# Kernel optimization log

Measured on AMD Instinct MI355X. Metric: run time of the kernel, lower is better.

Reference implementation:

```python
import jax, jax.numpy as jnp
import numpy as np

B, N, E, H = 4, 4096, 1024, 16
D = E // H            # head_dim = 64
P_DIM = 64            # proj_dim; feature dim = 2*P_DIM = 128
EPS = 1e-4


def setup_inputs() -> dict:
    key = jax.random.key(0)
    ks = jax.random.split(key, 9)
    x = jax.random.normal(ks[0], (B, N, E), jnp.float32)
    init = 0.02
    Wq = jax.random.normal(ks[1], (E, E), jnp.float32) * init
    Wk = jax.random.normal(ks[2], (E, E), jnp.float32) * init
    Wv = jax.random.normal(ks[3], (E, E), jnp.float32) * init
    Wo = jax.random.normal(ks[4], (E, E), jnp.float32) * init
    bq = jnp.zeros((E,), jnp.float32)
    bk = jnp.zeros((E,), jnp.float32)
    bv = jnp.zeros((E,), jnp.float32)
    bo = jnp.zeros((E,), jnp.float32)
    # orthogonal random projection matrix (proj_dim, head_dim), fixed (non-trainable)
    g = np.random.default_rng(0).normal(size=(P_DIM, D))
    P = jnp.asarray(np.linalg.qr(g)[0], jnp.float32)
    return dict(x=x, Wq=Wq, bq=bq, Wk=Wk, bk=bk, Wv=Wv, bv=bv, Wo=Wo, bo=bo, P=P)


def _heads(z):
    # (B, N, E) -> (B, H, N, D)
    return z.reshape(B, N, H, D).transpose(0, 2, 1, 3)


def _normalize(z):
    return z / (jnp.linalg.norm(z, axis=-1, keepdims=True) + EPS)


def reference(x, Wq, bq, Wk, bk, Wv, bv, Wo, bo, P):
    q = _heads(x @ Wq.T + bq)
    k = _heads(x @ Wk.T + bk)
    v = _heads(x @ Wv.T + bv)
    q = _normalize(q)
    k = _normalize(k)
    scale = H ** 0.25
    qp = jnp.einsum('bhnd,ed->bhne', q, P) * scale
    kp = jnp.einsum('bhnd,ed->bhne', k, P) * scale
    fscale = P_DIM ** (-0.5)   # x.shape[-1]**-0.5 with last dim = proj_dim
    qf = jnp.concatenate([jnp.sin(qp), jnp.cos(qp)], axis=-1) * fscale  # (B,H,N,2p)
    kf = jnp.concatenate([jnp.sin(kp), jnp.cos(kp)], axis=-1) * fscale
    # non-causal linear attention: q @ (k^T v)
    kv = jnp.einsum('bhme,bhmd->bhed', kf, v)          # (B,H,2p,D)
    o = jnp.einsum('bhne,bhed->bhnd', qf, kv)          # (B,H,N,D)
    o = o.transpose(0, 2, 1, 3).reshape(B, N, E)
    return o @ Wo.T + bo
```

## Files before the change

### kernel.cpp

```cpp
#include <hip/hip_runtime.h>
#include <hip/hip_bf16.h>
#include <stdint.h>


typedef __bf16 bf16x8 __attribute__((ext_vector_type(8)));
typedef float f32x4 __attribute__((ext_vector_type(4)));

#define AS1 __attribute__((address_space(1)))
#define AS3 __attribute__((address_space(3)))

__device__ __forceinline__ void gl2lds16(const void* g, void* l) {
    __builtin_amdgcn_global_load_lds((const AS1 void*)g, (AS3 void*)l, 16, 0, 0);
}

__global__ void detect_kernel(const unsigned short* __restrict__ x,
                              int* __restrict__ flag) {
    __shared__ int s;
    const int lane = threadIdx.x;
    if (lane == 0) s = 0;
    __syncthreads();
    int cnt = 0;
#pragma unroll
    for (int i = 0; i < 2; ++i) {
        const unsigned short u = x[i * 64 + lane];
        const int e = (u >> 7) & 0xFF;
        cnt += (e >= 117 && e <= 131) ? 1 : 0;
    }
    atomicAdd(&s, cnt);
    __syncthreads();
    if (lane == 0) *flag = (s >= 100) ? 1 : 0;
}

__global__ __launch_bounds__(256) void cvt_kernel(
    const void* __restrict__ src, __hip_bfloat16* __restrict__ dst,
    int n, const int* __restrict__ flag) {
    if (*flag) return;
    const int i = (blockIdx.x * 256 + threadIdx.x) * 8;
    if (i >= n) return;
    const float* s = (const float*)src + i;
    const float4 a = *(const float4*)s;
    const float4 b = *(const float4*)(s + 4);
    union { uint4 u; __hip_bfloat16 h[8]; } pk;
    pk.h[0] = __float2bfloat16(a.x); pk.h[1] = __float2bfloat16(a.y);
    pk.h[2] = __float2bfloat16(a.z); pk.h[3] = __float2bfloat16(a.w);
    pk.h[4] = __float2bfloat16(b.x); pk.h[5] = __float2bfloat16(b.y);
    pk.h[6] = __float2bfloat16(b.z); pk.h[7] = __float2bfloat16(b.w);
    *(uint4*)(dst + i) = pk.u;
}

static constexpr int GM = 16384, GN = 1024, GK = 1024;

__global__ __launch_bounds__(256) void gemm_bias_kernel(
    const void* __restrict__ Adirect,
    const __hip_bfloat16* __restrict__ Acvt,
    const void* __restrict__ W0r, const void* __restrict__ W1r,
    const void* __restrict__ W2r,
    const __hip_bfloat16* __restrict__ W0c, const __hip_bfloat16* __restrict__ W1c,
    const __hip_bfloat16* __restrict__ W2c,
    const void* __restrict__ b0r, const void* __restrict__ b1r,
    const void* __restrict__ b2r,
    void* __restrict__ o0, void* __restrict__ o1, void* __restrict__ o2,
    const int* __restrict__ flag, int last)
{
    __shared__ unsigned short smem[2 * 128 * 64];
    unsigned short* sA = smem;
    unsigned short* sB = smem + 128 * 64;

    const int tid  = threadIdx.x;
    const int lane = tid & 63;
    const int w    = tid >> 6;
    const int wm   = w >> 1, wn = w & 1;
    const int lr   = lane & 15, lk = lane >> 4;
    const int m0   = blockIdx.y * 128;
    const int n0   = blockIdx.x * 128;
    const int z    = blockIdx.z;
    const int fl   = *flag;

    const __hip_bfloat16* A = fl ? (const __hip_bfloat16*)Adirect : Acvt;
    const void* Wraw = (z == 0) ? W0r : (z == 1) ? W1r : W2r;
    const __hip_bfloat16* Wc = (z == 0) ? W0c : (z == 1) ? W1c : W2c;
    const __hip_bfloat16* W = fl ? (const __hip_bfloat16*)Wraw : Wc;
    const void* bias_raw = (z == 0) ? b0r : (z == 1) ? b1r : b2r;
    void* Cout = (z == 0) ? o0 : (z == 1) ? o1 : o2;

    f32x4 acc[4][4];
#pragma unroll
    for (int i = 0; i < 4; ++i)
#pragma unroll
        for (int j = 0; j < 4; ++j)
            acc[i][j] = (f32x4){0.f, 0.f, 0.f, 0.f};

    const __hip_bfloat16* Ab = A + (size_t)m0 * GK;
    const __hip_bfloat16* Wb = W + (size_t)n0 * GK;

    for (int k0 = 0; k0 < GK; k0 += 64) {
#pragma unroll
        for (int j = 0; j < 4; ++j) {
            const int chunk = j * 256 + tid;
            const int row   = chunk >> 3;
            const int c     = chunk & 7;
            const int cs    = c ^ (row & 7);
            gl2lds16(Ab + (size_t)row * GK + k0 + cs * 8,
                     (char*)sA + (j * 256 + w * 64) * 16);
            gl2lds16(Wb + (size_t)row * GK + k0 + cs * 8,
                     (char*)sB + (j * 256 + w * 64) * 16);
        }
        __syncthreads();
#pragma unroll
        for (int kk = 0; kk < 64; kk += 32) {
            const int jbase = kk >> 3;
            const int jj = (jbase + lk) ^ (lr & 7);
            bf16x8 af[4], bfr[4];
#pragma unroll
            for (int i = 0; i < 4; ++i)
                af[i] = *(const bf16x8*)&sA[(wm * 64 + i * 16 + lr) * 64 + jj * 8];
#pragma unroll
            for (int j = 0; j < 4; ++j)
                bfr[j] = *(const bf16x8*)&sB[(wn * 64 + j * 16 + lr) * 64 + jj * 8];
#pragma unroll
            for (int i = 0; i < 4; ++i)
#pragma unroll
                for (int j = 0; j < 4; ++j)
                    acc[i][j] = __builtin_amdgcn_mfma_f32_16x16x32_bf16(
                        af[i], bfr[j], acc[i][j], 0, 0, 0);
        }
        __syncthreads();
    }

    const bool f32out = (last != 0) && (fl == 0);
    if (f32out) {
#pragma unroll
        for (int j = 0; j < 4; ++j) {
            const int col = n0 + wn * 64 + j * 16 + lr;
            const float bv = ((const float*)bias_raw)[col];
#pragma unroll
            for (int i = 0; i < 4; ++i) {
                const int rbase = m0 + wm * 64 + i * 16 + lk * 4;
#pragma unroll
                for (int r = 0; r < 4; ++r)
                    ((float*)Cout)[(size_t)(rbase + r) * GN + col] = acc[i][j][r] + bv;
            }
        }
        return;
    }
    __hip_bfloat16* sC = (__hip_bfloat16*)smem;
#pragma unroll
    for (int j = 0; j < 4; ++j) {
        const int col = wn * 64 + j * 16 + lr;
        const float bv = fl ? __bfloat162float(((const __hip_bfloat16*)bias_raw)[n0 + col])
                            : ((const float*)bias_raw)[n0 + col];
        const int c2 = col >> 3, o = col & 7;
#pragma unroll
        for (int i = 0; i < 4; ++i) {
            const int rb = wm * 64 + i * 16 + lk * 4;
#pragma unroll
            for (int r = 0; r < 4; ++r) {
                const int row = rb + r;
                const int c2s = c2 ^ (row & 7);
                sC[row * 128 + c2s * 8 + o] = __float2bfloat16(acc[i][j][r] + bv);
            }
        }
    }
    __syncthreads();
    {
        const int row = tid >> 1, hf = tid & 1;
        __hip_bfloat16* dst = (__hip_bfloat16*)Cout + (size_t)(m0 + row) * GN + n0 + hf * 64;
#pragma unroll
        for (int q = 0; q < 8; ++q) {
            const int cc = (hf * 8 + q) ^ (row & 7);
            *(uint4*)(dst + q * 8) = *(const uint4*)&sC[row * 128 + cc * 8];
        }
    }
}

__device__ __forceinline__ void load_P(const void* Praw, int f,
                                       __hip_bfloat16* sP, int tid) {
    const int e = tid >> 2, q = tid & 3;
    union { uint4 u[2]; __hip_bfloat16 h[16]; } pk;
    if (f) {
        pk.u[0] = *(const uint4*)((const __hip_bfloat16*)Praw + e * 64 + q * 16);
        pk.u[1] = *(const uint4*)((const __hip_bfloat16*)Praw + e * 64 + q * 16 + 8);
    } else {
        const float* ps = (const float*)Praw + e * 64 + q * 16;
#pragma unroll
        for (int j = 0; j < 16; ++j) pk.h[j] = __float2bfloat16(ps[j]);
    }
    *(uint4*)&sP[e * 72 + q * 16]     = pk.u[0];
    *(uint4*)&sP[e * 72 + q * 16 + 8] = pk.u[1];
}

__global__ __launch_bounds__(256) void kv_kernel(
    const __hip_bfloat16* __restrict__ Km,
    const __hip_bfloat16* __restrict__ Vm,
    const void* __restrict__ Praw,
    float* __restrict__ gKV,
    const int* __restrict__ flag)
{
    __shared__ __hip_bfloat16 sK[64 * 72];
    __shared__ __hip_bfloat16 sVT[64 * 72];
    __shared__ __hip_bfloat16 sP[64 * 72];
    __shared__ __hip_bfloat16 sKFT[128 * 72];
    __shared__ float sRN[64];

    const int tid  = threadIdx.x;
    const int lane = tid & 63;
    const int w    = tid >> 6;
    const int lr   = lane & 15, lk = lane >> 4;
    const int bh   = blockIdx.y;
    const int b    = bh >> 4, h = bh & 15;
    const int nst  = blockIdx.x * 512;
    const int f    = *flag;

    load_P(Praw, f, sP, tid);

    f32x4 acck[2][4];
#pragma unroll
    for (int i = 0; i < 2; ++i)
#pragma unroll
        for (int j = 0; j < 4; ++j)
            acck[i][j] = (f32x4){0.f, 0.f, 0.f, 0.f};

    for (int s = 0; s < 8; ++s) {
        const int gn0 = nst + s * 64;
        __syncthreads();
        {
            const int n = tid >> 2, q = tid & 3;
            const size_t base = ((size_t)(b * 4096 + gn0 + n)) * 1024 + h * 64 + q * 16;
            uint4 k0 = *(const uint4*)(Km + base);
            uint4 k1 = *(const uint4*)(Km + base + 8);
            *(uint4*)&sK[n * 72 + q * 16]     = k0;
            *(uint4*)&sK[n * 72 + q * 16 + 8] = k1;
            union { uint4 u[2]; __hip_bfloat16 h[16]; } vv;
            vv.u[0] = *(const uint4*)(Vm + base);
            vv.u[1] = *(const uint4*)(Vm + base + 8);
#pragma unroll
            for (int j = 0; j < 16; ++j) sVT[(q * 16 + j) * 72 + n] = vv.h[j];
        }
        __syncthreads();
        {
            const int tl = lane >> 2, q2 = lane & 3;
            const int token = w * 16 + tl;
            union { bf16x8 v; __hip_bfloat16 h[8]; } a0, a1;
            a0.v = *(const bf16x8*)&sK[token * 72 + q2 * 16];
            a1.v = *(const bf16x8*)&sK[token * 72 + q2 * 16 + 8];
            float ss = 0.f;
#pragma unroll
            for (int j = 0; j < 8; ++j) {
                float x0 = __bfloat162float(a0.h[j]); ss += x0 * x0;
                float x1 = __bfloat162float(a1.h[j]); ss += x1 * x1;
            }
            ss += __shfl_xor(ss, 1, 64);
            ss += __shfl_xor(ss, 2, 64);
            if (q2 == 0) sRN[token] = 2.0f / (sqrtf(ss) + 1e-4f);
        }
        __syncthreads();
        {
            bf16x8 afr0 = *(const bf16x8*)&sK[(w * 16 + lr) * 72 + lk * 8];
            bf16x8 afr1 = *(const bf16x8*)&sK[(w * 16 + lr) * 72 + 32 + lk * 8];
            float rn[4];
#pragma unroll
            for (int r = 0; r < 4; ++r) rn[r] = sRN[w * 16 + lk * 4 + r];
#pragma unroll
            for (int eb = 0; eb < 4; ++eb) {
                f32x4 pa = (f32x4){0.f, 0.f, 0.f, 0.f};
                bf16x8 b0 = *(const bf16x8*)&sP[(eb * 16 + lr) * 72 + lk * 8];
                bf16x8 b1 = *(const bf16x8*)&sP[(eb * 16 + lr) * 72 + 32 + lk * 8];
                pa = __builtin_amdgcn_mfma_f32_16x16x32_bf16(afr0, b0, pa, 0, 0, 0);
                pa = __builtin_amdgcn_mfma_f32_16x16x32_bf16(afr1, b1, pa, 0, 0, 0);
                const int col = eb * 16 + lr;
#pragma unroll
                for (int r = 0; r < 4; ++r) {
                    const int row = w * 16 + lk * 4 + r;
                    float sv, cv;
                    __sincosf(pa[r] * rn[r], &sv, &cv);
                    sKFT[col * 72 + row]        = __float2bfloat16(sv * 0.125f);
                    sKFT[(col + 64) * 72 + row] = __float2bfloat16(cv * 0.125f);
                }
            }
        }
        __syncthreads();
#pragma unroll
        for (int ks = 0; ks < 2; ++ks) {
            bf16x8 a2[2], b2[4];
            a2[0] = *(const bf16x8*)&sKFT[(w * 16 + lr) * 72 + ks * 32 + lk * 8];
            a2[1] = *(const bf16x8*)&sKFT[((w + 4) * 16 + lr) * 72 + ks * 32 + lk * 8];
#pragma unroll
            for (int db = 0; db < 4; ++db)
                b2[db] = *(const bf16x8*)&sVT[(db * 16 + lr) * 72 + ks * 32 + lk * 8];
#pragma unroll
            for (int i = 0; i < 2; ++i)
#pragma unroll
                for (int db = 0; db < 4; ++db)
                    acck[i][db] = __builtin_amdgcn_mfma_f32_16x16x32_bf16(
                        a2[i], b2[db], acck[i][db], 0, 0, 0);
        }
    }

    float* out = gKV + (size_t)bh * 8192;
#pragma unroll
    for (int i = 0; i < 2; ++i)
#pragma unroll
        for (int db = 0; db < 4; ++db)
#pragma unroll
            for (int r = 0; r < 4; ++r) {
                const int e = (w + 4 * i) * 16 + lk * 4 + r;
                const int d = db * 16 + lr;
                atomicAdd(out + e * 64 + d, acck[i][db][r]);
            }
}

__global__ __launch_bounds__(256) void o_kernel(
    const __hip_bfloat16* __restrict__ Qm,
    const void* __restrict__ Praw,
    const float* __restrict__ gKV,
    __hip_bfloat16* __restrict__ O,
    const int* __restrict__ flag)
{
    __shared__ __hip_bfloat16 sQ[64 * 72];
    __shared__ __hip_bfloat16 sP[64 * 72];
    __shared__ __hip_bfloat16 sQF[64 * 136];
    __shared__ __hip_bfloat16 sKVT[64 * 136];
    __shared__ float sRN[64];

    const int tid  = threadIdx.x;
    const int lane = tid & 63;
    const int w    = tid >> 6;
    const int lr   = lane & 15, lk = lane >> 4;
    const int bh   = blockIdx.y;
    const int b    = bh >> 4, h = bh & 15;
    const int nst  = blockIdx.x * 256;
    const int f    = *flag;

    load_P(Praw, f, sP, tid);
    {
        const float* kvsrc = gKV + (size_t)bh * 8192;
        for (int t = tid; t < 8192; t += 256) {
            const int e = t >> 6, d = t & 63;
            sKVT[d * 136 + e] = __float2bfloat16(kvsrc[t]);
        }
    }

    for (int s = 0; s < 4; ++s) {
        const int gn0 = nst + s * 64;
        __syncthreads();
        {
            const int n = tid >> 2, q = tid & 3;
            const size_t base = ((size_t)(b * 4096 + gn0 + n)) * 1024 + h * 64 + q * 16;
            uint4 q0 = *(const uint4*)(Qm + base);
            uint4 q1 = *(const uint4*)(Qm + base + 8);
            *(uint4*)&sQ[n * 72 + q * 16]     = q0;
            *(uint4*)&sQ[n * 72 + q * 16 + 8] = q1;
        }
        __syncthreads();
        {
            const int tl = lane >> 2, q2 = lane & 3;
            const int token = w * 16 + tl;
            union { bf16x8 v; __hip_bfloat16 h[8]; } a0, a1;
            a0.v = *(const bf16x8*)&sQ[token * 72 + q2 * 16];
            a1.v = *(const bf16x8*)&sQ[token * 72 + q2 * 16 + 8];
            float ss = 0.f;
#pragma unroll
            for (int j = 0; j < 8; ++j) {
                float x0 = __bfloat162float(a0.h[j]); ss += x0 * x0;
                float x1 = __bfloat162float(a1.h[j]); ss += x1 * x1;
            }
            ss += __shfl_xor(ss, 1, 64);
            ss += __shfl_xor(ss, 2, 64);
            if (q2 == 0) sRN[token] = 2.0f / (sqrtf(ss) + 1e-4f);
        }
        __syncthreads();
        {
            bf16x8 afr0 = *(const bf16x8*)&sQ[(w * 16 + lr) * 72 + lk * 8];
            bf16x8 afr1 = *(const bf16x8*)&sQ[(w * 16 + lr) * 72 + 32 + lk * 8];
            float rn[4];
#pragma unroll
            for (int r = 0; r < 4; ++r) rn[r] = sRN[w * 16 + lk * 4 + r];
#pragma unroll
            for (int eb = 0; eb < 4; ++eb) {
                f32x4 pa = (f32x4){0.f, 0.f, 0.f, 0.f};
                bf16x8 b0 = *(const bf16x8*)&sP[(eb * 16 + lr) * 72 + lk * 8];
                bf16x8 b1 = *(const bf16x8*)&sP[(eb * 16 + lr) * 72 + 32 + lk * 8];
                pa = __builtin_amdgcn_mfma_f32_16x16x32_bf16(afr0, b0, pa, 0, 0, 0);
                pa = __builtin_amdgcn_mfma_f32_16x16x32_bf16(afr1, b1, pa, 0, 0, 0);
                const int col = eb * 16 + lr;
#pragma unroll
                for (int r = 0; r < 4; ++r) {
                    const int row = w * 16 + lk * 4 + r;
                    float sv, cv;
                    __sincosf(pa[r] * rn[r], &sv, &cv);
                    sQF[row * 136 + col]      = __float2bfloat16(sv * 0.125f);
                    sQF[row * 136 + 64 + col] = __float2bfloat16(cv * 0.125f);
                }
            }
        }
        __syncthreads();
        f32x4 oacc[4];
#pragma unroll
        for (int nb = 0; nb < 4; ++nb) oacc[nb] = (f32x4){0.f, 0.f, 0.f, 0.f};
#pragma unroll
        for (int ks = 0; ks < 4; ++ks) {
            bf16x8 aa = *(const bf16x8*)&sQF[(w * 16 + lr) * 136 + ks * 32 + lk * 8];
#pragma unroll
            for (int nb = 0; nb < 4; ++nb) {
                bf16x8 bb = *(const bf16x8*)&sKVT[(nb * 16 + lr) * 136 + ks * 32 + lk * 8];
                oacc[nb] = __builtin_amdgcn_mfma_f32_16x16x32_bf16(aa, bb, oacc[nb], 0, 0, 0);
            }
        }
#pragma unroll
        for (int nb = 0; nb < 4; ++nb)
#pragma unroll
            for (int r = 0; r < 4; ++r)
                sQ[(w * 16 + lk * 4 + r) * 72 + nb * 16 + lr] =
                    __float2bfloat16(oacc[nb][r]);
        __syncthreads();
        {
            const int n = tid >> 2, q = tid & 3;
            uint4 o0 = *(uint4*)&sQ[n * 72 + q * 16];
            uint4 o1 = *(uint4*)&sQ[n * 72 + q * 16 + 8];
            const size_t obase = ((size_t)(b * 4096 + gn0 + n)) * 1024 + h * 64 + q * 16;
            *(uint4*)(O + obase)     = o0;
            *(uint4*)(O + obase + 8) = o1;
        }
    }
}

extern "C" void kernel_launch(void* const* d_in, const int* in_sizes, int n_in,
                              void* d_out, int out_size, void* d_ws, size_t ws_size,
                              hipStream_t stream)
{
    (void)in_sizes; (void)n_in; (void)out_size;
    const void* x  = d_in[0];
    const void* Wq = d_in[1];
    const void* bq = d_in[2];
    const void* Wk = d_in[3];
    const void* bk = d_in[4];
    const void* Wv = d_in[5];
    const void* bv = d_in[6];
    const void* Wo = d_in[7];
    const void* bo = d_in[8];
    const void* P  = d_in[9];

    constexpr size_t XE = (size_t)GM * GN;
    constexpr size_t WE = (size_t)GN * GK;
    constexpr size_t KVE = (size_t)64 * 128 * 64;

    __hip_bfloat16* xb  = (__hip_bfloat16*)d_ws;
    __hip_bfloat16* wqb = xb + XE;
    __hip_bfloat16* wkb = wqb + WE;
    __hip_bfloat16* wvb = wkb + WE;
    __hip_bfloat16* wob = wvb + WE;
    __hip_bfloat16* R1  = wob + WE;
    __hip_bfloat16* R2  = R1 + XE;
    __hip_bfloat16* R3  = R2 + XE;

    const size_t need_fused = ((4 * XE + 4 * WE) * 2 + KVE * 4 + 256);
    const bool fused = ws_size >= need_fused;

    float* gKV;
    int* flag;
    if (fused) {
        gKV = (float*)(R3 + XE);
        flag = (int*)(gKV + KVE);
    } else {
        gKV = (float*)(R2 + XE);
        flag = (int*)(gKV + KVE);
    }

    dim3 blk(256);
    hipLaunchKernelGGL(detect_kernel, dim3(1), dim3(64), 0, stream,
                       (const unsigned short*)x, flag);
    hipMemsetAsync(gKV, 0, KVE * sizeof(float), stream);

    hipLaunchKernelGGL(cvt_kernel, dim3(8192), blk, 0, stream, x,  xb,  (int)XE, flag);
    hipLaunchKernelGGL(cvt_kernel, dim3(512),  blk, 0, stream, Wq, wqb, (int)WE, flag);
    hipLaunchKernelGGL(cvt_kernel, dim3(512),  blk, 0, stream, Wk, wkb, (int)WE, flag);
    hipLaunchKernelGGL(cvt_kernel, dim3(512),  blk, 0, stream, Wv, wvb, (int)WE, flag);
    hipLaunchKernelGGL(cvt_kernel, dim3(512),  blk, 0, stream, Wo, wob, (int)WE, flag);

    if (fused) {
        hipLaunchKernelGGL(gemm_bias_kernel, dim3(GN / 128, GM / 128, 3), blk, 0, stream,
                           x, xb, Wk, Wv, Wq, wkb, wvb, wqb, bk, bv, bq,
                           R1, R2, R3, flag, 0);
        hipLaunchKernelGGL(kv_kernel, dim3(8, 64), blk, 0, stream, R1, R2, P, gKV, flag);
        hipLaunchKernelGGL(o_kernel, dim3(16, 64), blk, 0, stream, R3, P, gKV, R1, flag);
        hipLaunchKernelGGL(gemm_bias_kernel, dim3(GN / 128, GM / 128, 1), blk, 0, stream,
                           R1, R1, Wo, Wo, Wo, wob, wob, wob, bo, bo, bo,
                           d_out, d_out, d_out, flag, 1);
    } else {
        dim3 gg(GN / 128, GM / 128, 1);
        hipLaunchKernelGGL(gemm_bias_kernel, gg, blk, 0, stream,
                           x, xb, Wk, Wk, Wk, wkb, wkb, wkb, bk, bk, bk,
                           R1, R1, R1, flag, 0);
        hipLaunchKernelGGL(gemm_bias_kernel, gg, blk, 0, stream,
                           x, xb, Wv, Wv, Wv, wvb, wvb, wvb, bv, bv, bv,
                           R2, R2, R2, flag, 0);
        hipLaunchKernelGGL(kv_kernel, dim3(8, 64), blk, 0, stream, R1, R2, P, gKV, flag);
        hipLaunchKernelGGL(gemm_bias_kernel, gg, blk, 0, stream,
                           x, xb, Wq, Wq, Wq, wqb, wqb, wqb, bq, bq, bq,
                           R2, R2, R2, flag, 0);
        hipLaunchKernelGGL(o_kernel, dim3(16, 64), blk, 0, stream, R2, P, gKV, R1, flag);
        hipLaunchKernelGGL(gemm_bias_kernel, gg, blk, 0, stream,
                           R1, R1, Wo, Wo, Wo, wob, wob, wob, bo, bo, bo,
                           d_out, d_out, d_out, flag, 1);
    }
}
```

Measured before the change: 426.4 us.

## Remap GEMM blocks per XCD, prefetch K/V/Q tiles in registers, double kv grid

The GEMM grid becomes 1D and block ids are remapped so that each XCD (id & 7) handles a contiguous band of M rows. This is meant to improve L2 reuse of A tiles within each chiplet. The kv and o kernels now load the next 64-token tile into registers while the current one is processed. They also compute the row norm straight from those registers, which removes one __syncthreads and a round trip through LDS. The kv kernel processes 256 tokens per block over twice as many blocks, raising parallelism at the cost of more atomic accumulation into gKV.

New measurement: 413.1 us. 1.03x faster.

```diff
diff --git a/kernel.cpp b/kernel.cpp
--- a/kernel.cpp
+++ b/kernel.cpp
@@ -71,10 +71,16 @@
     const int w    = tid >> 6;
     const int wm   = w >> 1, wn = w & 1;
     const int lr   = lane & 15, lk = lane >> 4;
-    const int m0   = blockIdx.y * 128;
-    const int n0   = blockIdx.x * 128;
-    const int z    = blockIdx.z;
-    const int fl   = *flag;
+
+    const int id    = blockIdx.x;
+    const int xcd   = id & 7;
+    const int slot  = id >> 3;
+    const int mslot = slot & 15;
+    const int rest  = slot >> 4;
+    const int m0    = (xcd * 16 + mslot) * 128;
+    const int n0    = (rest & 7) * 128;
+    const int z     = rest >> 3;
+    const int fl    = *flag;
 
     const __hip_bfloat16* A = fl ? (const __hip_bfloat16*)Adirect : Acvt;
     const void* Wraw = (z == 0) ? W0r : (z == 1) ? W1r : W2r;
@@ -187,6 +193,18 @@
     }
     *(uint4*)&sP[e * 72 + q * 16]     = pk.u[0];
     *(uint4*)&sP[e * 72 + q * 16 + 8] = pk.u[1];
+}
+
+__device__ __forceinline__ float sumsq16(uint4 a, uint4 b) {
+    union { uint4 u; __hip_bfloat16 h[8]; } x0, x1;
+    x0.u = a; x1.u = b;
+    float ss = 0.f;
+#pragma unroll
+    for (int j = 0; j < 8; ++j) {
+        float v0 = __bfloat162float(x0.h[j]); ss += v0 * v0;
+        float v1 = __bfloat162float(x1.h[j]); ss += v1 * v1;
+    }
+    return ss;
 }
 
 __global__ __launch_bounds__(256) void kv_kernel(
@@ -208,8 +226,9 @@
     const int lr   = lane & 15, lk = lane >> 4;
     const int bh   = blockIdx.y;
     const int b    = bh >> 4, h = bh & 15;
-    const int nst  = blockIdx.x * 512;
+    const int nst  = blockIdx.x * 256;
     const int f    = *flag;
+    const int n    = tid >> 2, q2 = tid & 3;
 
     load_P(Praw, f, sP, tid);
 
@@ -220,38 +239,30 @@
         for (int j = 0; j < 4; ++j)
             acck[i][j] = (f32x4){0.f, 0.f, 0.f, 0.f};
 
-    for (int s = 0; s < 8; ++s) {
-        const int gn0 = nst + s * 64;
-        __syncthreads();
+    size_t base = ((size_t)(b * 4096 + nst + n)) * 1024 + h * 64 + q2 * 16;
+    uint4 ka = *(const uint4*)(Km + base), kb = *(const uint4*)(Km + base + 8);
+    uint4 va = *(const uint4*)(Vm + base), vb = *(const uint4*)(Vm + base + 8);
+
+    for (int s = 0; s < 4; ++s) {
+        __syncthreads();
+        *(uint4*)&sK[n * 72 + q2 * 16]     = ka;
+        *(uint4*)&sK[n * 72 + q2 * 16 + 8] = kb;
         {
-            const int n = tid >> 2, q = tid & 3;
-            const size_t base = ((size_t)(b * 4096 + gn0 + n)) * 1024 + h * 64 + q * 16;
-            uint4 k0 = *(const uint4*)(Km + base);
-            uint4 k1 = *(const uint4*)(Km + base + 8);
-            *(uint4*)&sK[n * 72 + q * 16]     = k0;
-            *(uint4*)&sK[n * 72 + q * 16 + 8] = k1;
             union { uint4 u[2]; __hip_bfloat16 h[16]; } vv;
-            vv.u[0] = *(const uint4*)(Vm + base);
-            vv.u[1] = *(const uint4*)(Vm + base + 8);
-#pragma unroll
-            for (int j = 0; j < 16; ++j) sVT[(q * 16 + j) * 72 + n] = vv.h[j];
-        }
-        __syncthreads();
+            vv.u[0] = va; vv.u[1] = vb;
+#pragma unroll
+            for (int j = 0; j < 16; ++j) sVT[(q2 * 16 + j) * 72 + n] = vv.h[j];
+        }
         {
-            const int tl = lane >> 2, q2 = lane & 3;
-            const int token = w * 16 + tl;
-            union { bf16x8 v; __hip_bfloat16 h[8]; } a0, a1;
-            a0.v = *(const bf16x8*)&sK[token * 72 + q2 * 16];
-            a1.v = *(const bf16x8*)&sK[token * 72 + q2 * 16 + 8];
-            float ss = 0.f;
-#pragma unroll
-            for (int j = 0; j < 8; ++j) {
-                float x0 = __bfloat162float(a0.h[j]); ss += x0 * x0;
-                float x1 = __bfloat162float(a1.h[j]); ss += x1 * x1;
-            }
+            float ss = sumsq16(ka, kb);
             ss += __shfl_xor(ss, 1, 64);
             ss += __shfl_xor(ss, 2, 64);
-            if (q2 == 0) sRN[token] = 2.0f / (sqrtf(ss) + 1e-4f);
+            if (q2 == 0) sRN[n & 63] = 2.0f / (sqrtf(ss) + 1e-4f);
+        }
+        if (s < 3) {
+            base = ((size_t)(b * 4096 + nst + (s + 1) * 64 + n)) * 1024 + h * 64 + q2 * 16;
+            ka = *(const uint4*)(Km + base); kb = *(const uint4*)(Km + base + 8);
+            va = *(const uint4*)(Vm + base); vb = *(const uint4*)(Vm + base + 8);
         }
         __syncthreads();
         {
@@ -330,6 +341,7 @@
     const int b    = bh >> 4, h = bh & 15;
     const int nst  = blockIdx.x * 256;
     const int f    = *flag;
+    const int n    = tid >> 2, q2 = tid & 3;
 
     load_P(Praw, f, sP, tid);
     {
@@ -340,33 +352,23 @@
         }
     }
 
+    size_t base = ((size_t)(b * 4096 + nst + n)) * 1024 + h * 64 + q2 * 16;
+    uint4 qa = *(const uint4*)(Qm + base), qb = *(const uint4*)(Qm + base + 8);
+
     for (int s = 0; s < 4; ++s) {
         const int gn0 = nst + s * 64;
         __syncthreads();
+        *(uint4*)&sQ[n * 72 + q2 * 16]     = qa;
+        *(uint4*)&sQ[n * 72 + q2 * 16 + 8] = qb;
         {
-            const int n = tid >> 2, q = tid & 3;
-            const size_t base = ((size_t)(b * 4096 + gn0 + n)) * 1024 + h * 64 + q * 16;
-            uint4 q0 = *(const uint4*)(Qm + base);
-            uint4 q1 = *(const uint4*)(Qm + base + 8);
-            *(uint4*)&sQ[n * 72 + q * 16]     = q0;
-            *(uint4*)&sQ[n * 72 + q * 16 + 8] = q1;
-        }
-        __syncthreads();
-        {
-            const int tl = lane >> 2, q2 = lane & 3;
-            const int token = w * 16 + tl;
-            union { bf16x8 v; __hip_bfloat16 h[8]; } a0, a1;
-            a0.v = *(const bf16x8*)&sQ[token * 72 + q2 * 16];
-            a1.v = *(const bf16x8*)&sQ[token * 72 + q2 * 16 + 8];
-            float ss = 0.f;
-#pragma unroll
-            for (int j = 0; j < 8; ++j) {
-                float x0 = __bfloat162float(a0.h[j]); ss += x0 * x0;
-                float x1 = __bfloat162float(a1.h[j]); ss += x1 * x1;
-            }
+            float ss = sumsq16(qa, qb);
             ss += __shfl_xor(ss, 1, 64);
             ss += __shfl_xor(ss, 2, 64);
-            if (q2 == 0) sRN[token] = 2.0f / (sqrtf(ss) + 1e-4f);
+            if (q2 == 0) sRN[n & 63] = 2.0f / (sqrtf(ss) + 1e-4f);
+        }
+        if (s < 3) {
+            base = ((size_t)(b * 4096 + nst + (s + 1) * 64 + n)) * 1024 + h * 64 + q2 * 16;
+            qa = *(const uint4*)(Qm + base); qb = *(const uint4*)(Qm + base + 8);
         }
         __syncthreads();
         {
@@ -414,10 +416,9 @@
                     __float2bfloat16(oacc[nb][r]);
         __syncthreads();
         {
-            const int n = tid >> 2, q = tid & 3;
-            uint4 o0 = *(uint4*)&sQ[n * 72 + q * 16];
-            uint4 o1 = *(uint4*)&sQ[n * 72 + q * 16 + 8];
-            const size_t obase = ((size_t)(b * 4096 + gn0 + n)) * 1024 + h * 64 + q * 16;
+            uint4 o0 = *(uint4*)&sQ[n * 72 + q2 * 16];
+            uint4 o1 = *(uint4*)&sQ[n * 72 + q2 * 16 + 8];
+            const size_t obase = ((size_t)(b * 4096 + gn0 + n)) * 1024 + h * 64 + q2 * 16;
             *(uint4*)(O + obase)     = o0;
             *(uint4*)(O + obase + 8) = o1;
         }
@@ -478,28 +479,27 @@
     hipLaunchKernelGGL(cvt_kernel, dim3(512),  blk, 0, stream, Wo, wob, (int)WE, flag);
 
     if (fused) {
-        hipLaunchKernelGGL(gemm_bias_kernel, dim3(GN / 128, GM / 128, 3), blk, 0, stream,
+        hipLaunchKernelGGL(gemm_bias_kernel, dim3(3072), blk, 0, stream,
                            x, xb, Wk, Wv, Wq, wkb, wvb, wqb, bk, bv, bq,
                            R1, R2, R3, flag, 0);
-        hipLaunchKernelGGL(kv_kernel, dim3(8, 64), blk, 0, stream, R1, R2, P, gKV, flag);
+        hipLaunchKernelGGL(kv_kernel, dim3(16, 64), blk, 0, stream, R1, R2, P, gKV, flag);
         hipLaunchKernelGGL(o_kernel, dim3(16, 64), blk, 0, stream, R3, P, gKV, R1, flag);
-        hipLaunchKernelGGL(gemm_bias_kernel, dim3(GN / 128, GM / 128, 1), blk, 0, stream,
+        hipLaunchKernelGGL(gemm_bias_kernel, dim3(1024), blk, 0, stream,
                            R1, R1, Wo, Wo, Wo, wob, wob, wob, bo, bo, bo,
                            d_out, d_out, d_out, flag, 1);
     } else {
-        dim3 gg(GN / 128, GM / 128, 1);
-        hipLaunchKernelGGL(gemm_bias_kernel, gg, blk, 0, stream,
+        hipLaunchKernelGGL(gemm_bias_kernel, dim3(1024), blk, 0, stream,
                            x, xb, Wk, Wk, Wk, wkb, wkb, wkb, bk, bk, bk,
                            R1, R1, R1, flag, 0);
-        hipLaunchKernelGGL(gemm_bias_kernel, gg, blk, 0, stream,
+        hipLaunchKernelGGL(gemm_bias_kernel, dim3(1024), blk, 0, stream,
                            x, xb, Wv, Wv, Wv, wvb, wvb, wvb, bv, bv, bv,
                            R2, R2, R2, flag, 0);
-        hipLaunchKernelGGL(kv_kernel, dim3(8, 64), blk, 0, stream, R1, R2, P, gKV, flag);
-        hipLaunchKernelGGL(gemm_bias_kernel, gg, blk, 0, stream,
+        hipLaunchKernelGGL(kv_kernel, dim3(16, 64), blk, 0, stream, R1, R2, P, gKV, flag);
+        hipLaunchKernelGGL(gemm_bias_kernel, dim3(1024), blk, 0, stream,
                            x, xb, Wq, Wq, Wq, wqb, wqb, wqb, bq, bq, bq,
                            R2, R2, R2, flag, 0);
         hipLaunchKernelGGL(o_kernel, dim3(16, 64), blk, 0, stream, R2, P, gKV, R1, flag);
-        hipLaunchKernelGGL(gemm_bias_kernel, gg, blk, 0, stream,
+        hipLaunchKernelGGL(gemm_bias_kernel, dim3(1024), blk, 0, stream,
                            R1, R1, Wo, Wo, Wo, wob, wob, wob, bo, bo, bo,
                            d_out, d_out, d_out, flag, 1);
     }
```
